# Kernel tuning notes

Measured on AMD Instinct MI355X. Metric: run time of the kernel, lower is better.

Reference implementation:

```python
import jax, jax.numpy as jnp
import numpy as np

B, L, H = 128, 2048, 256


def setup_inputs() -> dict:
    key = jax.random.key(0)
    ks = jax.random.split(key, 9)
    s_in = 1.0 / np.sqrt(3.0)
    s_h = 1.0 / np.sqrt(H)
    return {
        "x": jax.random.normal(ks[0], (B, L, 3), dtype=jnp.float32),
        "Wp": jax.random.normal(ks[1], (3, H), dtype=jnp.float32) * s_in,
        "bp": jnp.zeros((H,), dtype=jnp.float32),
        "Wz": jax.random.normal(ks[2], (H, H), dtype=jnp.float32) * s_h,
        "bz": jnp.zeros((H,), dtype=jnp.float32),
        "Wh": jax.random.normal(ks[3], (H, H), dtype=jnp.float32) * s_h,
        "bh": jnp.zeros((H,), dtype=jnp.float32),
        "Wg": jax.random.normal(ks[4], (H, 1), dtype=jnp.float32) * s_h,
        "bg": jnp.zeros((1,), dtype=jnp.float32),
    }


def reference(x, Wp, bp, Wz, bz, Wh, bh, Wg, bg):
    # Precompute all per-timestep gate inputs with large batched GEMMs.
    inp = jnp.einsum("bli,ih->blh", x, Wp) + bp            # (B, L, H)
    z = jax.nn.sigmoid(jnp.einsum("blh,hk->blk", inp, Wz) + bz)   # update gate
    h_tilde = jnp.tanh(jnp.einsum("blh,hk->blk", inp, Wh) + bh)   # candidate

    # Sequential recurrence: h_t = (1 - z_t) * h_{t-1} + z_t * h_tilde_t.
    # pred_t = gauss_head(h_{t-1})  (pred is emitted BEFORE the state update).
    def step(h, zt_ht):
        zt, htl = zt_ht                      # each (B, H)
        pred = h @ Wg + bg                   # (B, 1) from previous state
        h_new = (1.0 - zt) * h + zt * htl
        return h_new, pred

    h0 = jnp.zeros((x.shape[0], Wz.shape[1]), dtype=x.dtype)
    zT = jnp.swapaxes(z, 0, 1)               # (L, B, H)
    hT = jnp.swapaxes(h_tilde, 0, 1)         # (L, B, H)
    _, preds = jax.lax.scan(step, h0, (zT, hT))
    preds = jnp.swapaxes(preds, 0, 1)        # (B, L, 1)
    return preds
```

## Files before the change

kernel.cpp:

```cpp
#include <hip/hip_runtime.h>

#define NB 128
#define NL 2048
#define NH 256
#define NSEG 16
#define SEGLEN (NL / NSEG)
#define RCHUNK 32
#define PBPITCH 17
#define PLANE (NB * NL)
#define CHUNK 32
#define NCHUNK (NL / CHUNK)
#define WORDS (CHUNK * 3)

typedef float f32x2 __attribute__((ext_vector_type(2)));
typedef __fp16 f16x2 __attribute__((ext_vector_type(2)));

__device__ __forceinline__ float fexp2(float v) { return __builtin_amdgcn_exp2f(v); }
__device__ __forceinline__ float frcp(float v)  { return __builtin_amdgcn_rcpf(v); }

__device__ __forceinline__ f32x2 pkfma(f32x2 a, f32x2 b, f32x2 c) {
#if __has_builtin(__builtin_elementwise_fma)
    return __builtin_elementwise_fma(a, b, c);
#else
    f32x2 r; r.x = fmaf(a.x, b.x, c.x); r.y = fmaf(a.y, b.y, c.y); return r;
#endif
}
__device__ __forceinline__ f32x2 splat2(float v) { f32x2 r; r.x = v; r.y = v; return r; }

union U32H2 { unsigned int u; f16x2 h; };

__global__ __launch_bounds__(256) void transpose_x(
        const float* __restrict__ x, float* __restrict__ xT) {
    const int gid = blockIdx.x * 256 + threadIdx.x;
    const float4* x4 = (const float4*)x;
    const float4 v0 = x4[gid * 3 + 0];
    const float4 v1 = x4[gid * 3 + 1];
    const float4 v2 = x4[gid * 3 + 2];
    const float4 p0 = {v0.x, v0.w, v1.z, v2.y};
    const float4 p1 = {v0.y, v1.x, v1.w, v2.z};
    const float4 p2 = {v0.z, v1.y, v2.x, v2.w};
    ((float4*)(xT + 0 * PLANE))[gid] = p0;
    ((float4*)(xT + 1 * PLANE))[gid] = p1;
    ((float4*)(xT + 2 * PLANE))[gid] = p2;
}

__global__ __launch_bounds__(256) void fold_kernel(
        const float* __restrict__ Wp, const float* __restrict__ bp,
        const float* __restrict__ Wz, const float* __restrict__ bz,
        const float* __restrict__ Wh, const float* __restrict__ bh,
        float* __restrict__ wsW) {
    const int tid = threadIdx.x;
    const int jj = tid & 15;
    const int hs = tid >> 4;
    const int j = blockIdx.x * 16 + jj;
    float mz0 = 0.f, mz1 = 0.f, mz2 = 0.f, cz = 0.f;
    float mh0 = 0.f, mh1 = 0.f, mh2 = 0.f, ch = 0.f;
#pragma unroll
    for (int i = 0; i < 16; ++i) {
        const int h = hs * 16 + i;
        const float wz = Wz[h * NH + j];
        const float wh = Wh[h * NH + j];
        const float p0 = Wp[h];
        const float p1 = Wp[NH + h];
        const float p2 = Wp[2 * NH + h];
        const float bb = bp[h];
        mz0 = fmaf(p0, wz, mz0); mz1 = fmaf(p1, wz, mz1); mz2 = fmaf(p2, wz, mz2);
        cz  = fmaf(bb, wz, cz);
        mh0 = fmaf(p0, wh, mh0); mh1 = fmaf(p1, wh, mh1); mh2 = fmaf(p2, wh, mh2);
        ch  = fmaf(bb, wh, ch);
    }
    __shared__ float red[256][9];
    red[tid][0] = mz0; red[tid][1] = mz1; red[tid][2] = mz2; red[tid][3] = cz;
    red[tid][4] = mh0; red[tid][5] = mh1; red[tid][6] = mh2; red[tid][7] = ch;
    __syncthreads();
    if (tid < 16) {
        float v[8];
#pragma unroll
        for (int k = 0; k < 8; ++k) {
            float a = 0.f;
#pragma unroll
            for (int g = 0; g < 16; ++g) a += red[g * 16 + tid][k];
            v[k] = a;
        }
        v[3] += bz[j];
        v[7] += bh[j];
        const float SZ = -1.4426950408889634f;
        const float SH = -2.8853900817779268f;
        float4* w4 = (float4*)(wsW + j * 8);
        w4[0] = make_float4(v[0] * SZ, v[1] * SZ, v[2] * SZ, v[3] * SZ);
        w4[1] = make_float4(v[4] * SH, v[5] * SH, v[6] * SH, v[7] * SH);
    }
}

#define GATE2(XQ, U0, AV, BV)                                                   \
    {                                                                           \
        const float* xf_ = (const float*)(XQ);                                  \
        const f32x2 xx_ = *(const f32x2*)&xf_[2*(U0)];                          \
        const f32x2 xy_ = *(const f32x2*)&xf_[8 + 2*(U0)];                      \
        const f32x2 xz_ = *(const f32x2*)&xf_[16 + 2*(U0)];                     \
        const f32x2 s1_ = pkfma(xx_, wax, pkfma(xy_, way, pkfma(xz_, waz, waw)));\
        const f32x2 s2_ = pkfma(xx_, wbx, pkfma(xy_, wby, pkfma(xz_, wbz, wbw)));\
        f32x2 e1_, e2_;                                                         \
        e1_.x = fexp2(s1_.x); e1_.y = fexp2(s1_.y);                             \
        e2_.x = fexp2(s2_.x); e2_.y = fexp2(s2_.y);                             \
        const f32x2 q_  = pkfma(e1_, e2_, e1_);                                 \
        f32x2 den_ = q_ + e2_;                                                  \
        den_ = den_ + 1.f;                                                      \
        f32x2 rr_; rr_.x = frcp(den_.x); rr_.y = frcp(den_.y);                  \
        AV = q_ * rr_;                                          \
        BV = (1.f - e2_) * rr_;                                 \
    }

#define LOAD8(XQ, SC)                                                           \
    {                                                                           \
        XQ[0] = p04[(SC) * 2];     XQ[1] = p04[(SC) * 2 + 1];                   \
        XQ[2] = p14[(SC) * 2];     XQ[3] = p14[(SC) * 2 + 1];                   \
        XQ[4] = p24[(SC) * 2];     XQ[5] = p24[(SC) * 2 + 1];                   \
    }

__global__ __launch_bounds__(256, 8) void pass1_seg(
        const float* __restrict__ xT, const float* __restrict__ wsW,
        float* __restrict__ Aarr, float* __restrict__ Barr) {
    const int tid = threadIdx.x;
    const int b = blockIdx.x >> 4;
    const int s = blockIdx.x & (NSEG - 1);
    if (s == NSEG - 1) return;

    const float4* wv = (const float4*)(wsW + tid * 8);
    const float4 wA4 = wv[0];
    const float4 wB4 = wv[1];
    const f32x2 wax = splat2(wA4.x), way = splat2(wA4.y), waz = splat2(wA4.z), waw = splat2(wA4.w);
    const f32x2 wbx = splat2(wB4.x), wby = splat2(wB4.y), wbz = splat2(wB4.z), wbw = splat2(wB4.w);

    const int base = b * NL + s * SEGLEN;
    const float4* p04 = (const float4*)(xT + 0 * PLANE + base);
    const float4* p14 = (const float4*)(xT + 1 * PLANE + base);
    const float4* p24 = (const float4*)(xT + 2 * PLANE + base);

#define P1_BODY(XQ)                                                             \
    _Pragma("unroll")                                                           \
    for (int u0 = 0; u0 < 4; ++u0) {                                            \
        f32x2 av, bv;                                                           \
        GATE2(XQ, u0, av, bv);                                                  \
        Bacc = fmaf(av.x, Bacc, bv.x);                                          \
        Bacc = fmaf(av.y, Bacc, bv.y);                                          \
        Apk *= av;                                                              \
    }

    f32x2 Apk = { 1.f, 1.f };
    float Bacc = 0.f;
    float4 xa[6], xb[6];
    LOAD8(xa, 0);
    for (int c = 0; c < 8; ++c) {
        LOAD8(xb, 2 * c + 1);
        P1_BODY(xa);
        const int nxt = (c < 7) ? (2 * c + 2) : 0;
        LOAD8(xa, nxt);
        P1_BODY(xb);
    }
    const size_t o = ((size_t)b * NSEG + s) * NH + tid;
    Aarr[o] = Apk.x * Apk.y;
    Barr[o] = Bacc;
#undef P1_BODY
}

__global__ __launch_bounds__(256, 8) void pass3_pred(
        const float* __restrict__ xT, const float* __restrict__ wsW,
        const float* __restrict__ Wg, const float* __restrict__ bg,
        const float* __restrict__ Aarr, const float* __restrict__ Barr,
        float* __restrict__ out) {
    const int tid = threadIdx.x;
    const int b = blockIdx.x >> 4;
    const int s = blockIdx.x & (NSEG - 1);

    const float4* wv = (const float4*)(wsW + tid * 8);
    const float4 wA4 = wv[0];
    const float4 wB4 = wv[1];
    const f32x2 wax = splat2(wA4.x), way = splat2(wA4.y), waz = splat2(wA4.z), waw = splat2(wA4.w);
    const f32x2 wbx = splat2(wB4.x), wby = splat2(wB4.y), wbz = splat2(wB4.z), wbw = splat2(wB4.w);
    const float wg = Wg[tid];
    const f32x2 wgpk = splat2(wg);
    const float bgv = bg[0];

    float h = 0.f;
    {
        const size_t pbase = (size_t)b * NSEG * NH + tid;
        for (int k0 = 0; k0 < s; k0 += 8) {
            float Ak[8], Bk[8];
#pragma unroll
            for (int k = 0; k < 8; ++k) {
                const int kk = k0 + k;
                const bool u = kk < s;
                Ak[k] = u ? Aarr[pbase + (size_t)kk * NH] : 1.f;
                Bk[k] = u ? Barr[pbase + (size_t)kk * NH] : 0.f;
            }
#pragma unroll
            for (int k = 0; k < 8; ++k) h = fmaf(Ak[k], h, Bk[k]);
        }
    }
    float g = h * wg;

    const int base = b * NL + s * SEGLEN;
    const float4* p04 = (const float4*)(xT + 0 * PLANE + base);
    const float4* p14 = (const float4*)(xT + 1 * PLANE + base);
    const float4* p24 = (const float4*)(xT + 2 * PLANE + base);

    __shared__ unsigned int pbuf[NH * PBPITCH];
    __shared__ unsigned int part2[16 * PBPITCH];

    const int q   = tid & 15;
    const int grp = tid >> 4;

#define P3_BODY(XQ, Q0)                                                         \
    _Pragma("unroll")                                                           \
    for (int u0 = 0; u0 < 4; ++u0) {                                            \
        f32x2 av, bv;                                                           \
        GATE2(XQ, u0, av, bv);                                                  \
        const f32x2 bw = bv * wgpk;                                             \
        const float p0_ = g;                 \
        g = fmaf(av.x, g, bw.x);                                                \
        const float p1_ = g;                                                    \
        g = fmaf(av.y, g, bw.y);                                                \
        U32H2 pk_; pk_.h = __builtin_amdgcn_cvt_pkrtz(p0_, p1_);                \
        pbuf[tid * PBPITCH + (Q0) + u0] = pk_.u;                                \
    }

    float4 xa[6], xb[6];
    LOAD8(xa, 0);
    for (int c2 = 0; c2 < 4; ++c2) {
        LOAD8(xb, 4 * c2 + 1);
        P3_BODY(xa, 0);
        LOAD8(xa, 4 * c2 + 2);
        P3_BODY(xb, 4);
        LOAD8(xb, 4 * c2 + 3);
        P3_BODY(xa, 8);
        {
            const int nxt = (c2 < 3) ? (4 * c2 + 4) : 0;
            LOAD8(xa, nxt);
        }
        P3_BODY(xb, 12);
        __syncthreads();
        {
            f16x2 acc2 = (f16x2)0.f;
#pragma unroll
            for (int j = 0; j < 16; ++j) {
                U32H2 rd; rd.u = pbuf[(grp * 16 + j) * PBPITCH + q];
                acc2 += rd.h;
            }
            U32H2 wr; wr.h = acc2;
            part2[grp * PBPITCH + q] = wr.u;
        }
        __syncthreads();
        if (tid < 16) {
            f16x2 a3 = (f16x2)0.f;
#pragma unroll
            for (int g2 = 0; g2 < 16; ++g2) {
                U32H2 rd; rd.u = part2[g2 * PBPITCH + tid];
                a3 += rd.h;
            }
            float2 o2;
            o2.x = (float)a3.x + bgv;
            o2.y = (float)a3.y + bgv;
            *(float2*)&out[(size_t)b * NL + (size_t)s * SEGLEN + c2 * RCHUNK + 2 * tid] = o2;
        }
    }
#undef P3_BODY
}

__global__ __launch_bounds__(256) void scan_kernel_nows(
        const float* __restrict__ x, const float* __restrict__ wsW,
        const float* __restrict__ Wg, const float* __restrict__ bg,
        float* __restrict__ out) {
    const int tid  = threadIdx.x;
    const int lane = tid & 63;
    const int wid  = tid >> 6;
    const int b = blockIdx.x;

    const float4* wv = (const float4*)(wsW + tid * 8);
    const float4 wA = wv[0];
    const float4 wB = wv[1];
    const float  wg = Wg[tid];
    const float  bgv = bg[0];

    const float* xb = x + (size_t)b * (NL * 3);

    __shared__ float4 xbuf[2][CHUNK];
    __shared__ float  predbuf[2][4][CHUNK];
    float* xbf = (float*)xbuf;

    const int sw = tid;
    const int sidx = (sw / 3) * 4 + (sw % 3);

    if (tid < WORDS) xbf[sidx] = xb[sw];
    __syncthreads();

    float h = 0.f;
    for (int c = 0; c < NCHUNK; ++c) {
        const int cur = c & 1;
        float nv = 0.f;
        if (tid < WORDS && c + 1 < NCHUNK) nv = xb[(c + 1) * WORDS + sw];

        float p[CHUNK];
        const float4* xc = xbuf[cur];
#pragma unroll
        for (int t = 0; t < CHUNK; ++t) {
            const float4 xv = xc[t];
            const float e1 = fexp2(fmaf(xv.x, wA.x, fmaf(xv.y, wA.y, fmaf(xv.z, wA.z, wA.w))));
            const float e2 = fexp2(fmaf(xv.x, wB.x, fmaf(xv.y, wB.y, fmaf(xv.z, wB.z, wB.w))));
            const float d2 = 1.f + e2;
            const float e1d2 = e1 * d2;
            const float r  = frcp(e1d2 + d2);
            p[t] = h * wg;
            h = fmaf(e1d2 * r, h, (1.f - e2) * r);
        }
#pragma unroll
        for (int t = 0; t < CHUNK; ++t) {
            float v = p[t];
            v += __shfl_xor(v, 1, 64);
            v += __shfl_xor(v, 2, 64);
            v += __shfl_xor(v, 4, 64);
            v += __shfl_xor(v, 8, 64);
            v += __shfl_xor(v, 16, 64);
            v += __shfl_xor(v, 32, 64);
            p[t] = v;
        }
        if (lane == 0) {
            float4* dpr = (float4*)&predbuf[cur][wid][0];
#pragma unroll
            for (int j2 = 0; j2 < CHUNK / 4; ++j2)
                dpr[j2] = make_float4(p[4*j2], p[4*j2+1], p[4*j2+2], p[4*j2+3]);
        }
        if (tid < WORDS && c + 1 < NCHUNK) xbf[(cur ^ 1) * CHUNK * 4 + sidx] = nv;
        __syncthreads();
        if (tid < CHUNK) {
            const float ssum = predbuf[cur][0][tid] + predbuf[cur][1][tid]
                             + predbuf[cur][2][tid] + predbuf[cur][3][tid];
            out[(size_t)b * NL + c * CHUNK + tid] = ssum + bgv;
        }
    }
}

extern "C" void kernel_launch(void* const* d_in, const int* in_sizes, int n_in,
                              void* d_out, int out_size, void* d_ws, size_t ws_size,
                              hipStream_t stream) {
    const float* x  = (const float*)d_in[0];
    const float* Wp = (const float*)d_in[1];
    const float* bp = (const float*)d_in[2];
    const float* Wz = (const float*)d_in[3];
    const float* bz = (const float*)d_in[4];
    const float* Wh = (const float*)d_in[5];
    const float* bh = (const float*)d_in[6];
    const float* Wg = (const float*)d_in[7];
    const float* bg = (const float*)d_in[8];
    float* out = (float*)d_out;

    float* wsW = (float*)d_ws;
    float* Aarr = wsW + 8 * NH;
    float* Barr = Aarr + (size_t)NB * NSEG * NH;
    float* xTp  = Barr + (size_t)NB * NSEG * NH;

    const size_t need = ((size_t)(8 * NH) + 2 * (size_t)NB * NSEG * NH
                        + 3 * (size_t)PLANE) * sizeof(float);

    fold_kernel<<<16, 256, 0, stream>>>(Wp, bp, Wz, bz, Wh, bh, wsW);

    if (ws_size >= need) {
        transpose_x<<<PLANE / 4 / 256, 256, 0, stream>>>(x, xTp);
        pass1_seg<<<NB * NSEG, 256, 0, stream>>>(xTp, wsW, Aarr, Barr);
        pass3_pred<<<NB * NSEG, 256, 0, stream>>>(xTp, wsW, Wg, bg, Aarr, Barr, out);
    } else {
        scan_kernel_nows<<<NB, 256, 0, stream>>>(x, wsW, Wg, bg, out);
    }
}
```

Before: 75.79 us.

## Batch LDS prediction stores as 64-bit and share one reciprocal per pair

Result: slower. 85.81 us (+13.2%).

```diff
diff --git a/kernel.cpp b/kernel.cpp
--- a/kernel.cpp
+++ b/kernel.cpp
@@ -6,7 +6,7 @@
 #define NSEG 16
 #define SEGLEN (NL / NSEG)
 #define RCHUNK 32
-#define PBPITCH 17
+#define PB2PITCH 9
 #define PLANE (NB * NL)
 #define CHUNK 32
 #define NCHUNK (NL / CHUNK)
@@ -92,8 +92,7 @@
     }
 }
 
-#define GATE2(XQ, U0, AV, BV)                                                   \
-    {                                                                           \
+#define GATE2_CORE(XQ, U0)                                                      \
         const float* xf_ = (const float*)(XQ);                                  \
         const f32x2 xx_ = *(const f32x2*)&xf_[2*(U0)];                          \
         const f32x2 xy_ = *(const f32x2*)&xf_[8 + 2*(U0)];                      \
@@ -103,13 +102,11 @@
         f32x2 e1_, e2_;                                                         \
         e1_.x = fexp2(s1_.x); e1_.y = fexp2(s1_.y);                             \
         e2_.x = fexp2(s2_.x); e2_.y = fexp2(s2_.y);                             \
-        const f32x2 q_  = pkfma(e1_, e2_, e1_);                                 \
+        const f32x2 q_ = pkfma(e1_, e2_, e1_);                                  \
         f32x2 den_ = q_ + e2_;                                                  \
         den_ = den_ + 1.f;                                                      \
-        f32x2 rr_; rr_.x = frcp(den_.x); rr_.y = frcp(den_.y);                  \
-        AV = q_ * rr_;                                          \
-        BV = (1.f - e2_) * rr_;                                 \
-    }
+        const float rp_ = frcp(den_.x * den_.y);                                \
+        f32x2 rr_; rr_.x = den_.y * rp_; rr_.y = den_.x * rp_;
 
 #define LOAD8(XQ, SC)                                                           \
     {                                                                           \
@@ -140,8 +137,9 @@
 #define P1_BODY(XQ)                                                             \
     _Pragma("unroll")                                                           \
     for (int u0 = 0; u0 < 4; ++u0) {                                            \
-        f32x2 av, bv;                                                           \
-        GATE2(XQ, u0, av, bv);                                                  \
+        GATE2_CORE(XQ, u0);                                                     \
+        const f32x2 av = q_ * rr_;                              \
+        const f32x2 bv = (1.f - e2_) * rr_;                     \
         Bacc = fmaf(av.x, Bacc, bv.x);                                          \
         Bacc = fmaf(av.y, Bacc, bv.y);                                          \
         Apk *= av;                                                              \
@@ -180,6 +178,7 @@
     const f32x2 wbx = splat2(wB4.x), wby = splat2(wB4.y), wbz = splat2(wB4.z), wbw = splat2(wB4.w);
     const float wg = Wg[tid];
     const f32x2 wgpk = splat2(wg);
+    const f32x2 mwgpk = splat2(-wg);
     const float bgv = bg[0];
 
     float h = 0.f;
@@ -205,27 +204,28 @@
     const float4* p14 = (const float4*)(xT + 1 * PLANE + base);
     const float4* p24 = (const float4*)(xT + 2 * PLANE + base);
 
-    __shared__ unsigned int pbuf[NH * PBPITCH];
-    __shared__ unsigned int part2[16 * PBPITCH];
-
-    const int q   = tid & 15;
-    const int grp = tid >> 4;
+    __shared__ uint2 pbuf2[NH * PB2PITCH];
+    __shared__ uint2 part2[16 * PB2PITCH];
+
+    const int qh   = tid & 7;
+    const int grp  = tid >> 3;
 
 #define P3_BODY(XQ, Q0)                                                         \
     _Pragma("unroll")                                                           \
     for (int u0 = 0; u0 < 4; ++u0) {                                            \
-        f32x2 av, bv;                                                           \
-        GATE2(XQ, u0, av, bv);                                                  \
-        const f32x2 bw = bv * wgpk;                                             \
+        GATE2_CORE(XQ, u0);                                                     \
+        const f32x2 av = q_ * rr_;                                              \
+        const f32x2 bw = pkfma(e2_, mwgpk, wgpk) * rr_;          \
         const float p0_ = g;                 \
         g = fmaf(av.x, g, bw.x);                                                \
         const float p1_ = g;                                                    \
         g = fmaf(av.y, g, bw.y);                                                \
         U32H2 pk_; pk_.h = __builtin_amdgcn_cvt_pkrtz(p0_, p1_);                \
-        pbuf[tid * PBPITCH + (Q0) + u0] = pk_.u;                                \
+        pk[(Q0) + u0] = pk_.u;                                                  \
     }
 
     float4 xa[6], xb[6];
+    unsigned int pk[16];
     LOAD8(xa, 0);
     for (int c2 = 0; c2 < 4; ++c2) {
         LOAD8(xb, 4 * c2 + 1);
@@ -239,23 +239,32 @@
             LOAD8(xa, nxt);
         }
         P3_BODY(xb, 12);
+#pragma unroll
+        for (int v = 0; v < 8; ++v)
+            pbuf2[tid * PB2PITCH + v] = make_uint2(pk[2 * v], pk[2 * v + 1]);
         __syncthreads();
-        {
-            f16x2 acc2 = (f16x2)0.f;
-#pragma unroll
-            for (int j = 0; j < 16; ++j) {
-                U32H2 rd; rd.u = pbuf[(grp * 16 + j) * PBPITCH + q];
-                acc2 += rd.h;
+        if (tid < 128) {
+            f16x2 aLo = (f16x2)0.f, aHi = (f16x2)0.f;
+#pragma unroll
+            for (int jj = 0; jj < 16; ++jj) {
+                const int j = (jj + grp) & 15;
+                const uint2 rd = pbuf2[(grp * 16 + j) * PB2PITCH + qh];
+                U32H2 lo; lo.u = rd.x;
+                U32H2 hi; hi.u = rd.y;
+                aLo += lo.h;
+                aHi += hi.h;
             }
-            U32H2 wr; wr.h = acc2;
-            part2[grp * PBPITCH + q] = wr.u;
+            U32H2 wLo; wLo.h = aLo;
+            U32H2 wHi; wHi.h = aHi;
+            part2[grp * PB2PITCH + qh] = make_uint2(wLo.u, wHi.u);
         }
         __syncthreads();
         if (tid < 16) {
+            const unsigned int* p2u = (const unsigned int*)part2;
             f16x2 a3 = (f16x2)0.f;
 #pragma unroll
             for (int g2 = 0; g2 < 16; ++g2) {
-                U32H2 rd; rd.u = part2[g2 * PBPITCH + tid];
+                U32H2 rd; rd.u = p2u[g2 * (2 * PB2PITCH) + tid];
                 a3 += rd.h;
             }
             float2 o2;
```
